# Performance work log

Hardware: AMD Instinct MI355X
Metric: run time of the kernel (lower is better)

Reference implementation:

```python
import jax, jax.numpy as jnp
import numpy as np

R = 3                 # corr_radius
STRIDE = 4
RES = (384, 512)      # model_resolution (H, W)
G = 2 * R + 1         # 7: support grid side


def setup_inputs() -> dict:
    key = jax.random.key(0)
    ks = jax.random.split(key, 16)
    B, S, N, C = 1, 8, 1024, 128
    H0, W0 = RES[0] // STRIDE, RES[1] // STRIDE  # 96, 128
    inp = {}
    for i in range(4):
        h, w = H0 >> i, W0 >> i
        inp[f"fmaps{i}"] = jax.random.normal(ks[i], (B, S, C, h, w), jnp.float32)
        inp[f"track{i}"] = jax.random.normal(ks[4 + i], (B, G * G, N, C), jnp.float32)
    inp["coords"] = jax.random.uniform(ks[8], (B, S, N, 2), jnp.float32) * jnp.asarray([W0 - 1.0, H0 - 1.0], jnp.float32)
    inp["vis"] = jax.random.normal(ks[9], (B, S, N, 1), jnp.float32)
    inp["conf"] = jax.random.normal(ks[10], (B, S, N, 1), jnp.float32)
    r2 = G * G
    inp["w1"] = jax.random.normal(ks[11], (r2 * r2, 384), jnp.float32) * (1.0 / np.sqrt(r2 * r2))
    inp["b1"] = jnp.zeros((384,), jnp.float32)
    inp["w2"] = jax.random.normal(ks[12], (384, 256), jnp.float32) * (1.0 / np.sqrt(384))
    inp["b2"] = jnp.zeros((256,), jnp.float32)
    inp["time_emb"] = jax.random.normal(ks[13], (1, S, 1110), jnp.float32) * 0.02
    return inp


def bilinear_sample(fmap, x, y):
    """fmap: (BT, C, H, W); x, y: (BT, M) pixel coords. Border padding, align_corners=True
    (matches torch grid_sample as used by co-tracker's bilinear_sampler)."""
    BT, C, H, W = fmap.shape
    x0f = jnp.floor(x)
    y0f = jnp.floor(y)
    wx = (x - x0f)[:, None, :]
    wy = (y - y0f)[:, None, :]
    x0 = jnp.clip(x0f.astype(jnp.int32), 0, W - 1)
    x1 = jnp.clip(x0f.astype(jnp.int32) + 1, 0, W - 1)
    y0 = jnp.clip(y0f.astype(jnp.int32), 0, H - 1)
    y1 = jnp.clip(y0f.astype(jnp.int32) + 1, 0, H - 1)
    flat = fmap.reshape(BT, C, H * W)

    def g(yi, xi):
        idx = (yi * W + xi)[:, None, :]  # (BT, 1, M)
        return jnp.take_along_axis(flat, idx, axis=2)  # (BT, C, M)

    return (g(y0, x0) * (1 - wx) * (1 - wy) + g(y0, x1) * wx * (1 - wy)
            + g(y1, x0) * (1 - wx) * wy + g(y1, x1) * wx * wy)


def posenc(x, min_deg=0, max_deg=10):
    scales = jnp.asarray([2.0 ** i for i in range(min_deg, max_deg)], x.dtype)
    xb = (x[..., None, :] * scales[:, None]).reshape(x.shape[:-1] + (-1,))
    four = jnp.sin(jnp.concatenate([xb, xb + 0.5 * jnp.pi], axis=-1))
    return jnp.concatenate([x, four], axis=-1)


def reference(fmaps0, fmaps1, fmaps2, fmaps3, track0, track1, track2, track3,
              coords, vis, conf, w1, b1, w2, b2, time_emb):
    B, S, N, _ = coords.shape
    fps = [fmaps0, fmaps1, fmaps2, fmaps3]
    tps = [track0, track1, track2, track3]
    d = jnp.linspace(-R, R, G)
    xoff, yoff = jnp.meshgrid(d, d, indexing='ij')  # (7,7): rows = x offset, cols = y offset

    embs = []
    for lvl in range(4):
        fm = fps[lvl]
        C, H, W = fm.shape[2], fm.shape[3], fm.shape[4]
        c = coords.reshape(B * S, N, 1, 1, 2) / (2.0 ** lvl)
        x = c[..., 0] + xoff          # (B*S, N, 7, 7)
        y = c[..., 1] + yoff
        M = N * G * G
        sampled = bilinear_sample(fm.reshape(B * S, C, H, W), x.reshape(B * S, M), y.reshape(B * S, M))
        corr_feat = sampled.reshape(B, S, C, N, G, G).transpose(0, 1, 3, 4, 5, 2)  # (B,S,N,7,7,C)
        track = tps[lvl].reshape(B, G, G, N, C).transpose(0, 3, 1, 2, 4)           # (B,N,7,7,C)
        vol = jnp.einsum('btnhwc,bnijc->btnhwij', corr_feat, track)                # (B,S,N,7,7,7,7)
        h = jax.nn.gelu(vol.reshape(B * S * N, G * G * G * G) @ w1 + b1, approximate=False)
        embs.append(h @ w2 + b2)
    corr_embs = jnp.concatenate(embs, axis=-1).reshape(B, S, N, -1)  # (B,S,N,1024)

    rel_f = jnp.pad(coords[:, :-1] - coords[:, 1:], ((0, 0), (0, 1), (0, 0), (0, 0)))
    rel_b = jnp.pad(coords[:, 1:] - coords[:, :-1], ((0, 0), (1, 0), (0, 0), (0, 0)))
    scale = jnp.asarray([RES[1], RES[0]], jnp.float32) / STRIDE
    rel_emb = posenc(jnp.concatenate([rel_f / scale, rel_b / scale], axis=-1))  # (B,S,N,84)

    x = jnp.concatenate([vis, conf, corr_embs, rel_emb], axis=-1)  # (B,S,N,1110)
    x = x.transpose(0, 2, 1, 3).reshape(B * N, S, -1) + time_emb
    return x.reshape(B, N, S, -1)
```

## Files before the change

kernel.cpp:

```cpp
#include <hip/hip_runtime.h>
#include <math.h>


#define SN 8
#define NN 1024
#define CC 128
#define K1P2 2752
#define H1 384
#define H2 256
#define DOUT 1110

typedef short bf16x8 __attribute__((ext_vector_type(8)));
typedef short s16x4 __attribute__((ext_vector_type(4)));
typedef float f32x4 __attribute__((ext_vector_type(4)));

__device__ inline unsigned short f2b(float x) {
    union { float f; unsigned u; } v; v.f = x;
    unsigned r = v.u + 0x7FFFu + ((v.u >> 16) & 1u);
    return (unsigned short)(r >> 16);
}
__device__ inline float b2f(unsigned short u) {
    union { unsigned u; float f; } v; v.u = (unsigned)u << 16; return v.f;
}
__device__ inline void gll16(const void* g, void* l) {
    __builtin_amdgcn_global_load_lds(
        (const __attribute__((address_space(1))) void*)g,
        (__attribute__((address_space(3))) void*)l, 16, 0, 0);
}
__device__ inline int swz(int row, int g) {
    return row * 128 + ((g ^ (row & 7)) << 3);
}

__global__ __launch_bounds__(256) void conv_fmap_kernel(
    const float* __restrict__ in, unsigned short* __restrict__ outp,
    int H, int W)
{
    const int Hp = H + 8, Wp = W + 8;
    const int s = blockIdx.x / Hp, yp = blockIdx.x % Hp;
    const int y = min(max(yp - 4, 0), H - 1);
    const float* src = in + (size_t)s * CC * H * W + (size_t)y * W;
    unsigned short* dst = outp + ((size_t)s * Hp + yp) * Wp * CC;
    for (int idx = threadIdx.x; idx < Wp * CC; idx += 256) {
        int xp = idx >> 7, c = idx & 127;
        int x = min(max(xp - 4, 0), W - 1);
        dst[idx] = f2b(src[(size_t)c * H * W + x]);
    }
}

__global__ __launch_bounds__(256, 3) void sample_vol_kernel(
    const unsigned short* __restrict__ fq0, const unsigned short* __restrict__ fq1,
    const unsigned short* __restrict__ fq2, const unsigned short* __restrict__ fq3,
    const float* __restrict__ tk0, const float* __restrict__ tk1,
    const float* __restrict__ tk2, const float* __restrict__ tk3,
    const float* __restrict__ coords,
    unsigned short* __restrict__ vol,
    int lv0)
{
    __shared__ __align__(16) unsigned short bufA[80 * 128];
    __shared__ __align__(16) unsigned short bufB[80 * 128];
    __shared__ __align__(16) unsigned short pcL[80 * 68];
    const int n = blockIdx.x & 1023, g = blockIdx.x >> 10;
    const int lvl = lv0 + g;
    const unsigned short* fpad = (lvl == 0) ? fq0 : (lvl == 1) ? fq1
                               : (lvl == 2) ? fq2 : fq3;
    const float* track = (lvl == 0) ? tk0 : (lvl == 1) ? tk1
                       : (lvl == 2) ? tk2 : tk3;
    const int Wp = (128 >> lvl) + 8;
    const int t = threadIdx.x;
    const int lane = t & 63, wv = t >> 6;
    const int rsub = lane & 15, kq = lane >> 4;
    const float inv = 1.0f / (float)(1 << lvl);
    const size_t plane = (size_t)((96 >> lvl) + 8) * Wp * CC;

    int poff[5], ldso[5];
    #pragma unroll
    for (int i = 0; i < 5; ++i) {
        int task64 = wv * 5 + i;
        int point = task64 * 4 + (lane >> 4);
        int v = point / 10, xs = point - v * 10;
        int j = (lane & 15) ^ (point & 7);
        poff[i] = (v * Wp + xs) * CC + j * 8;
        ldso[i] = task64 * 512;
    }

    float cxa[SN], cya[SN];
    int fxa[SN], fya[SN], ea[SN];
    #pragma unroll
    for (int s = 0; s < SN; ++s) {
        float2 c2 = *(const float2*)&coords[((size_t)s * NN + n) * 2];
        cxa[s] = c2.x * inv; cya[s] = c2.y * inv;
        fxa[s] = (int)floorf(cxa[s]);
        fya[s] = (int)floorf(cya[s]);
        ea[s] = (fxa[s] - 3) & ~1;
    }

    int p0b[2], ij0a[2], tau8[2]; bool vld[2];
    #pragma unroll
    for (int rep = 0; rep < 2; ++rep) {
        int tau = t + rep * 256;
        vld[rep] = (tau < 343);
        int tt = vld[rep] ? tau : 0;
        int ab = tt / 7, blk = tt - 7 * ab;
        int a = ab / 7, b = ab - 7 * a;
        p0b[rep] = b * 10 + a;
        ij0a[rep] = blk * 8;
        tau8[rep] = tt * 8;
    }

    {
        const unsigned short* base =
            fpad + ((fya[0] + 1) * Wp + (ea[0] + 4)) * CC;
        #pragma unroll
        for (int i = 0; i < 5; ++i) gll16(base + poff[i], &bufA[ldso[i]]);
    }
    for (int task = t; task < 49 * 16; task += 256) {
        int row = task >> 4, gg = task & 15;
        const float* srcp = &track[((size_t)row * NN + n) * CC + gg * 8];
        float4 f0 = *(const float4*)srcp;
        float4 f1 = *(const float4*)(srcp + 4);
        bf16x8 v8;
        v8[0] = f2b(f0.x); v8[1] = f2b(f0.y); v8[2] = f2b(f0.z); v8[3] = f2b(f0.w);
        v8[4] = f2b(f1.x); v8[5] = f2b(f1.y); v8[6] = f2b(f1.z); v8[7] = f2b(f1.w);
        *(bf16x8*)&bufB[swz(row, gg)] = v8;
    }
    {
        unsigned* T32 = (unsigned*)bufB;
        for (int i = t; i < 15 * 64; i += 256) T32[49 * 64 + i] = 0;
    }
    asm volatile("s_waitcnt lgkmcnt(0)" ::: "memory");
    __builtin_amdgcn_sched_barrier(0);
    __builtin_amdgcn_s_barrier();
    bf16x8 tf[4];
    #pragma unroll
    for (int kk = 0; kk < 4; ++kk)
        tf[kk] = *(const bf16x8*)&bufB[swz(wv * 16 + rsub, kk * 4 + kq)];
    asm volatile("s_waitcnt lgkmcnt(0)" ::: "memory");
    __builtin_amdgcn_sched_barrier(0);
    __builtin_amdgcn_s_barrier();
    __builtin_amdgcn_sched_barrier(0);
    {
        const unsigned short* base =
            fpad + plane + ((fya[1] + 1) * Wp + (ea[1] + 4)) * CC;
        #pragma unroll
        for (int i = 0; i < 5; ++i) gll16(base + poff[i], &bufB[ldso[i]]);
    }

    #pragma unroll
    for (int sl = 0; sl < SN; ++sl) {
        unsigned short* pbuf = (sl & 1) ? bufB : bufA;
        const float wx = cxa[sl] - (float)fxa[sl], wy = cya[sl] - (float)fya[sl];
        const float w00 = (1.f - wx) * (1.f - wy), w10 = wx * (1.f - wy);
        const float w01 = (1.f - wx) * wy,         w11 = wx * wy;
        const int off = fxa[sl] - 3 - ea[sl];

        if (sl == 0) {
            asm volatile("s_waitcnt vmcnt(5) lgkmcnt(0)" ::: "memory");
        } else if (sl == 1) {
            if (wv < 2) asm volatile("s_waitcnt vmcnt(7) lgkmcnt(0)" ::: "memory");
            else        asm volatile("s_waitcnt vmcnt(6) lgkmcnt(0)" ::: "memory");
        } else if (sl == SN - 1) {
            if (wv < 2) asm volatile("s_waitcnt vmcnt(4) lgkmcnt(0)" ::: "memory");
            else        asm volatile("s_waitcnt vmcnt(2) lgkmcnt(0)" ::: "memory");
        } else {
            if (wv < 2) asm volatile("s_waitcnt vmcnt(9) lgkmcnt(0)" ::: "memory");
            else        asm volatile("s_waitcnt vmcnt(7) lgkmcnt(0)" ::: "memory");
        }
        __builtin_amdgcn_sched_barrier(0);
        __builtin_amdgcn_s_barrier();
        __builtin_amdgcn_sched_barrier(0);

        {
            f32x4 acc[5] = {};
            __builtin_amdgcn_s_setprio(1);
            #pragma unroll
            for (int kk = 0; kk < 4; ++kk) {
                int gg = kk * 4 + kq;
                #pragma unroll
                for (int ti = 0; ti < 5; ++ti) {
                    bf16x8 a = *(const bf16x8*)&pbuf[swz(ti * 16 + rsub, gg)];
                    acc[ti] = __builtin_amdgcn_mfma_f32_16x16x32_bf16(a, tf[kk], acc[ti], 0, 0, 0);
                }
            }
            __builtin_amdgcn_s_setprio(0);
            const int col = wv * 16 + rsub;
            #pragma unroll
            for (int ti = 0; ti < 5; ++ti)
                #pragma unroll
                for (int r = 0; r < 4; ++r)
                    pcL[(ti * 16 + kq * 4 + r) * 68 + col] = f2b(acc[ti][r]);
        }
        asm volatile("s_waitcnt lgkmcnt(0)" ::: "memory");
        __builtin_amdgcn_s_barrier();
        __builtin_amdgcn_sched_barrier(0);

        if (sl + 2 < SN) {
            const unsigned short* base =
                fpad + (size_t)(sl + 2) * plane
                + ((fya[sl + 2] + 1) * Wp + (ea[sl + 2] + 4)) * CC;
            #pragma unroll
            for (int i = 0; i < 5; ++i) gll16(base + poff[i], &pbuf[ldso[i]]);
        }
        __builtin_amdgcn_sched_barrier(0);

        {
            unsigned short* vrow = vol + ((size_t)(g * SN + sl) * NN + n) * K1P2;
            #pragma unroll
            for (int rep = 0; rep < 2; ++rep) {
                if (vld[rep]) {
                    int base = (p0b[rep] + off) * 68 + ij0a[rep];
                    s16x4 a0 = *(const s16x4*)&pcL[base],       a1 = *(const s16x4*)&pcL[base + 4];
                    s16x4 b0 = *(const s16x4*)&pcL[base + 68],  b1 = *(const s16x4*)&pcL[base + 72];
                    s16x4 c0 = *(const s16x4*)&pcL[base + 680], c1 = *(const s16x4*)&pcL[base + 684];
                    s16x4 d0 = *(const s16x4*)&pcL[base + 748], d1 = *(const s16x4*)&pcL[base + 752];
                    unsigned w[4];
                    #pragma unroll
                    for (int j = 0; j < 4; ++j) {
                        const int e0 = 2 * j, e1 = 2 * j + 1;
                        float v0 = w00 * b2f((unsigned short)(e0 < 4 ? a0[e0 & 3] : a1[e0 & 3]))
                                 + w10 * b2f((unsigned short)(e0 < 4 ? b0[e0 & 3] : b1[e0 & 3]))
                                 + w01 * b2f((unsigned short)(e0 < 4 ? c0[e0 & 3] : c1[e0 & 3]))
                                 + w11 * b2f((unsigned short)(e0 < 4 ? d0[e0 & 3] : d1[e0 & 3]));
                        float v1 = w00 * b2f((unsigned short)(e1 < 4 ? a0[e1 & 3] : a1[e1 & 3]))
                                 + w10 * b2f((unsigned short)(e1 < 4 ? b0[e1 & 3] : b1[e1 & 3]))
                                 + w01 * b2f((unsigned short)(e1 < 4 ? c0[e1 & 3] : c1[e1 & 3]))
                                 + w11 * b2f((unsigned short)(e1 < 4 ? d0[e1 & 3] : d1[e1 & 3]));
                        w[j] = (unsigned)f2b(v0) | ((unsigned)f2b(v1) << 16);
                    }
                    uint4 st; st.x = w[0]; st.y = w[1]; st.z = w[2]; st.w = w[3];
                    *(uint4*)(vrow + tau8[rep]) = st;
                }
            }
        }
    }
}

__global__ __launch_bounds__(256) void zpad_kernel(
    unsigned short* __restrict__ vol, int rows)
{
    int r = blockIdx.x * 256 + threadIdx.x;
    if (r < rows) {
        uint4 z; z.x = 0; z.y = 0; z.z = 0; z.w = 0;
        *(uint4*)(vol + (size_t)r * K1P2 + 2744) = z;
    }
}

__global__ __launch_bounds__(256) void conv_w1_kernel(
    const float* __restrict__ w1, unsigned short* __restrict__ w1t)
{
    __shared__ float tile[32][33];
    const int kb = blockIdx.x * 32, nb = blockIdx.y * 32;
    const int tx = threadIdx.x & 31, ty = threadIdx.x >> 5;
    #pragma unroll
    for (int i = 0; i < 32; i += 8) {
        int kp = kb + ty + i;
        int k = -1;
        if (kp < 2744) {
            int tau = kp >> 3, r = kp & 7;
            int ab = tau / 7, blk = tau - 7 * ab;
            int ij = blk * 8 + r;
            if (ij < 49) k = ab * 49 + ij;
        }
        tile[ty + i][tx] = (k >= 0) ? w1[(size_t)k * H1 + nb + tx] : 0.f;
    }
    __syncthreads();
    #pragma unroll
    for (int i = 0; i < 32; i += 8)
        w1t[(size_t)(nb + ty + i) * K1P2 + kb + tx] = f2b(tile[tx][ty + i]);
}

__global__ __launch_bounds__(256, 3) void gemm1_kernel(
    const unsigned short* __restrict__ A,
    const unsigned short* __restrict__ Bt,
    const float* __restrict__ bias,
    unsigned short* __restrict__ Hout)
{
    __shared__ __align__(16) unsigned short As[3 * 128 * 32];
    __shared__ __align__(16) unsigned short Bs[3 * 128 * 32];
    const int h = blockIdx.x, q = gridDim.x >> 3;
    const int l = (h & 7) * q + (h >> 3);
    const int m0 = (l / 3) * 128, n0 = (l % 3) * 128;
    const int t = threadIdx.x, lane = t & 63, wv = t >> 6;
    const int wm = wv >> 1, wn = wv & 1;
    const int rsub = lane & 15, kq = lane >> 4;

    const int rA0 = t >> 2, sA0 = (t & 3) ^ ((rA0 >> 1) & 3);
    const int rA1 = (t + 256) >> 2, sA1 = ((t + 256) & 3) ^ ((rA1 >> 1) & 3);
    const unsigned short* gA0 = A  + (size_t)(m0 + rA0) * K1P2 + sA0 * 8;
    const unsigned short* gA1 = A  + (size_t)(m0 + rA1) * K1P2 + sA1 * 8;
    const unsigned short* gB0 = Bt + (size_t)(n0 + rA0) * K1P2 + sA0 * 8;
    const unsigned short* gB1 = Bt + (size_t)(n0 + rA1) * K1P2 + sA1 * 8;
    const int chunk0 = (t & ~63) * 8, chunk1 = (256 + (t & ~63)) * 8;

    f32x4 acc[4][4] = {};

    const int NSTEP = K1P2 / 32;
    #pragma unroll
    for (int p = 0; p < 2; ++p) {
        size_t ko = (size_t)p * 32;
        int lb = p * 4096;
        gll16(gA0 + ko, &As[lb + chunk0]); gll16(gA1 + ko, &As[lb + chunk1]);
        gll16(gB0 + ko, &Bs[lb + chunk0]); gll16(gB1 + ko, &Bs[lb + chunk1]);
    }
    int cur = 0, nxt = 2;
    for (int st = 0; st < NSTEP; ++st) {
        if (st + 1 < NSTEP) asm volatile("s_waitcnt vmcnt(4)" ::: "memory");
        else                asm volatile("s_waitcnt vmcnt(0)" ::: "memory");
        __builtin_amdgcn_s_barrier();
        __builtin_amdgcn_sched_barrier(0);
        if (st + 2 < NSTEP) {
            size_t ko = (size_t)(st + 2) * 32;
            int lb = nxt * 4096;
            gll16(gA0 + ko, &As[lb + chunk0]);
            gll16(gA1 + ko, &As[lb + chunk1]);
            gll16(gB0 + ko, &Bs[lb + chunk0]);
            gll16(gB1 + ko, &Bs[lb + chunk1]);
        }
        const int lb = cur * 4096;
        bf16x8 af[4], bfr[4];
        #pragma unroll
        for (int mi = 0; mi < 4; ++mi) {
            int r = wm * 64 + mi * 16 + rsub;
            int phys = r * 4 + (kq ^ ((r >> 1) & 3));
            af[mi] = *(const bf16x8*)&As[lb + phys * 8];
        }
        #pragma unroll
        for (int ni = 0; ni < 4; ++ni) {
            int r = wn * 64 + ni * 16 + rsub;
            int phys = r * 4 + (kq ^ ((r >> 1) & 3));
            bfr[ni] = *(const bf16x8*)&Bs[lb + phys * 8];
        }
        __builtin_amdgcn_s_setprio(1);
        #pragma unroll
        for (int mi = 0; mi < 4; ++mi)
            #pragma unroll
            for (int ni = 0; ni < 4; ++ni)
                acc[mi][ni] = __builtin_amdgcn_mfma_f32_16x16x32_bf16(
                    af[mi], bfr[ni], acc[mi][ni], 0, 0, 0);
        __builtin_amdgcn_s_setprio(0);
        cur = (cur == 2) ? 0 : cur + 1;
        nxt = (nxt == 2) ? 0 : nxt + 1;
    }
    #pragma unroll
    for (int mi = 0; mi < 4; ++mi) {
        int row = m0 + wm * 64 + mi * 16 + kq * 4;
        #pragma unroll
        for (int ni = 0; ni < 4; ++ni) {
            int col = n0 + wn * 64 + ni * 16 + rsub;
            float bcol = bias[col];
            #pragma unroll
            for (int r = 0; r < 4; ++r) {
                float x = acc[mi][ni][r] + bcol;
                float gg = 0.5f * x * (1.f + erff(x * 0.70710678118654752f));
                Hout[(size_t)(row + r) * H1 + col] = f2b(gg);
            }
        }
    }
}

__global__ __launch_bounds__(256, 3) void gemm2_kernel(
    const unsigned short* __restrict__ A,
    const unsigned short* __restrict__ Bt,
    const float* __restrict__ bias,
    const float* __restrict__ te,
    float* __restrict__ out,
    int lv0)
{
    __shared__ __align__(16) unsigned short As[3 * 128 * 32];
    __shared__ __align__(16) unsigned short Bs[3 * 128 * 32];
    const int h = blockIdx.x, q = gridDim.x >> 3;
    const int l = (h & 7) * q + (h >> 3);
    const int m0 = (l >> 1) * 128, n0 = (l & 1) * 128;
    const int t = threadIdx.x, lane = t & 63, wv = t >> 6;
    const int wm = wv >> 1, wn = wv & 1;
    const int rsub = lane & 15, kq = lane >> 4;

    const int rA0 = t >> 2, sA0 = (t & 3) ^ ((rA0 >> 1) & 3);
    const int rA1 = (t + 256) >> 2, sA1 = ((t + 256) & 3) ^ ((rA1 >> 1) & 3);
    const unsigned short* gA0 = A  + (size_t)(m0 + rA0) * H1 + sA0 * 8;
    const unsigned short* gA1 = A  + (size_t)(m0 + rA1) * H1 + sA1 * 8;
    const unsigned short* gB0 = Bt + (size_t)(n0 + rA0) * H1 + sA0 * 8;
    const unsigned short* gB1 = Bt + (size_t)(n0 + rA1) * H1 + sA1 * 8;
    const int chunk0 = (t & ~63) * 8, chunk1 = (256 + (t & ~63)) * 8;

    f32x4 acc[4][4] = {};

    const int NSTEP = H1 / 32;
    #pragma unroll
    for (int p = 0; p < 2; ++p) {
        size_t ko = (size_t)p * 32;
        int lb = p * 4096;
        gll16(gA0 + ko, &As[lb + chunk0]); gll16(gA1 + ko, &As[lb + chunk1]);
        gll16(gB0 + ko, &Bs[lb + chunk0]); gll16(gB1 + ko, &Bs[lb + chunk1]);
    }
    int cur = 0, nxt = 2;
    for (int st = 0; st < NSTEP; ++st) {
        if (st + 1 < NSTEP) asm volatile("s_waitcnt vmcnt(4)" ::: "memory");
        else                asm volatile("s_waitcnt vmcnt(0)" ::: "memory");
        __builtin_amdgcn_s_barrier();
        __builtin_amdgcn_sched_barrier(0);
        if (st + 2 < NSTEP) {
            size_t ko = (size_t)(st + 2) * 32;
            int lb = nxt * 4096;
            gll16(gA0 + ko, &As[lb + chunk0]);
            gll16(gA1 + ko, &As[lb + chunk1]);
            gll16(gB0 + ko, &Bs[lb + chunk0]);
            gll16(gB1 + ko, &Bs[lb + chunk1]);
        }
        const int lb = cur * 4096;
        bf16x8 af[4], bfr[4];
        #pragma unroll
        for (int mi = 0; mi < 4; ++mi) {
            int r = wm * 64 + mi * 16 + rsub;
            int phys = r * 4 + (kq ^ ((r >> 1) & 3));
            af[mi] = *(const bf16x8*)&As[lb + phys * 8];
        }
        #pragma unroll
        for (int ni = 0; ni < 4; ++ni) {
            int r = wn * 64 + ni * 16 + rsub;
            int phys = r * 4 + (kq ^ ((r >> 1) & 3));
            bfr[ni] = *(const bf16x8*)&Bs[lb + phys * 8];
        }
        __builtin_amdgcn_s_setprio(1);
        #pragma unroll
        for (int mi = 0; mi < 4; ++mi)
            #pragma unroll
            for (int ni = 0; ni < 4; ++ni)
                acc[mi][ni] = __builtin_amdgcn_mfma_f32_16x16x32_bf16(
                    af[mi], bfr[ni], acc[mi][ni], 0, 0, 0);
        __builtin_amdgcn_s_setprio(0);
        cur = (cur == 2) ? 0 : cur + 1;
        nxt = (nxt == 2) ? 0 : nxt + 1;
    }
    #pragma unroll
    for (int mi = 0; mi < 4; ++mi) {
        int rowb = m0 + wm * 64 + mi * 16 + kq * 4;
        #pragma unroll
        for (int ni = 0; ni < 4; ++ni) {
            int col = n0 + wn * 64 + ni * 16 + rsub;
            float bcol = bias[col];
            #pragma unroll
            for (int r = 0; r < 4; ++r) {
                int row = rowb + r;
                int g = row >> 13, s = (row >> 10) & 7, n = row & 1023;
                int dcol = 2 + (lv0 + g) * H2 + col;
                out[((size_t)n * SN + s) * DOUT + dcol] =
                    acc[mi][ni][r] + bcol + te[s * DOUT + dcol];
            }
        }
    }
}

__global__ __launch_bounds__(256) void conv_t_kernel(
    const float* __restrict__ in, unsigned short* __restrict__ outp,
    int K, int Nw, int Kp)
{
    __shared__ float tile[32][33];
    const int kb = blockIdx.x * 32, nb = blockIdx.y * 32;
    const int tx = threadIdx.x & 31, ty = threadIdx.x >> 5;
    #pragma unroll
    for (int i = 0; i < 32; i += 8) {
        int k = kb + ty + i, nn = nb + tx;
        tile[ty + i][tx] = (k < K && nn < Nw) ? in[(size_t)k * Nw + nn] : 0.f;
    }
    __syncthreads();
    #pragma unroll
    for (int i = 0; i < 32; i += 8) {
        int nn = nb + ty + i, k = kb + tx;
        if (nn < Nw) outp[(size_t)nn * Kp + k] = f2b(tile[tx][ty + i]);
    }
}

__global__ __launch_bounds__(128) void tail_kernel(
    const float* __restrict__ coords, const float* __restrict__ vis,
    const float* __restrict__ conf, const float* __restrict__ te,
    float* __restrict__ out)
{
    const int b = blockIdx.x;
    const int n = b >> 3, s = b & 7;
    const int d = threadIdx.x;
    if (d >= 86) return;
    const size_t ob = (size_t)b * DOUT;
    if (d == 0) {
        out[ob + 0] = vis[(size_t)s * NN + n] + te[s * DOUT + 0];
    } else if (d == 1) {
        out[ob + 1] = conf[(size_t)s * NN + n] + te[s * DOUT + 1];
    } else {
        int rd = d - 2;
        float cx = coords[((size_t)s * NN + n) * 2 + 0];
        float cy = coords[((size_t)s * NN + n) * 2 + 1];
        float rfx = 0.f, rfy = 0.f, rbx = 0.f, rby = 0.f;
        if (s < SN - 1) {
            rfx = cx - coords[((size_t)(s + 1) * NN + n) * 2 + 0];
            rfy = cy - coords[((size_t)(s + 1) * NN + n) * 2 + 1];
        }
        if (s > 0) {
            rbx = cx - coords[((size_t)(s - 1) * NN + n) * 2 + 0];
            rby = cy - coords[((size_t)(s - 1) * NN + n) * 2 + 1];
        }
        float r4[4] = {rfx / 128.f, rfy / 96.f, rbx / 128.f, rby / 96.f};
        float val;
        if (rd < 4) {
            val = r4[rd];
        } else if (rd < 44) {
            int q = rd - 4; int deg = q >> 2, comp = q & 3;
            val = sinf(r4[comp] * (float)(1 << deg));
        } else {
            int q = rd - 44; int deg = q >> 2, comp = q & 3;
            val = sinf(r4[comp] * (float)(1 << deg) + 1.57079632679489662f);
        }
        int od = 1026 + rd;
        out[ob + od] = val + te[s * DOUT + od];
    }
}

extern "C" void kernel_launch(void* const* d_in, const int* in_sizes, int n_in,
                              void* d_out, int out_size, void* d_ws, size_t ws_size,
                              hipStream_t stream) {
    const float* fmaps[4] = {(const float*)d_in[0], (const float*)d_in[2],
                             (const float*)d_in[4], (const float*)d_in[6]};
    const float* track[4] = {(const float*)d_in[1], (const float*)d_in[3],
                             (const float*)d_in[5], (const float*)d_in[7]};
    const float* coords = (const float*)d_in[8];
    const float* vis    = (const float*)d_in[9];
    const float* conf   = (const float*)d_in[10];
    const float* w1     = (const float*)d_in[11];
    const float* b1     = (const float*)d_in[12];
    const float* w2     = (const float*)d_in[13];
    const float* b2     = (const float*)d_in[14];
    const float* te     = (const float*)d_in[15];
    float* out = (float*)d_out;

    const int Hs[4] = {96, 48, 24, 12};
    const int Ws[4] = {128, 64, 32, 16};

    char* wsb = (char*)d_ws;
    unsigned short* w1t = (unsigned short*)wsb;
    size_t off = (size_t)H1 * K1P2 * 2;
    unsigned short* w2t = (unsigned short*)(wsb + off);
    off += (size_t)H2 * H1 * 2;
    unsigned short* fpad[4];
    for (int l = 0; l < 4; ++l) {
        fpad[l] = (unsigned short*)(wsb + off);
        off += (size_t)SN * (Hs[l] + 8) * (Ws[l] + 8) * CC * 2;
    }
    off += 512;
    const size_t fixed = off;
    int n_lv = 4;
    while (n_lv > 1 &&
           fixed + (size_t)n_lv * SN * NN * (K1P2 + H1) * 2 > ws_size)
        n_lv >>= 1;
    unsigned short* volb = (unsigned short*)(wsb + fixed);
    unsigned short* hb   = volb + (size_t)n_lv * SN * NN * K1P2;

    conv_w1_kernel<<<dim3(K1P2 / 32, H1 / 32), 256, 0, stream>>>(w1, w1t);
    conv_t_kernel<<<dim3(H1 / 32, H2 / 32), 256, 0, stream>>>(w2, w2t, H1, H2, H1);
    for (int l = 0; l < 4; ++l)
        conv_fmap_kernel<<<SN * (Hs[l] + 8), 256, 0, stream>>>(
            fmaps[l], fpad[l], Hs[l], Ws[l]);
    zpad_kernel<<<(n_lv * SN * NN + 255) / 256, 256, 0, stream>>>(
        volb, n_lv * SN * NN);

    for (int lv0 = 0; lv0 < 4; lv0 += n_lv) {
        sample_vol_kernel<<<n_lv * NN, 256, 0, stream>>>(
            fpad[0], fpad[1], fpad[2], fpad[3],
            track[0], track[1], track[2], track[3],
            coords, volb, lv0);
        const int rows = n_lv * SN * NN;
        gemm1_kernel<<<(rows / 128) * 3, 256, 0, stream>>>(volb, w1t, b1, hb);
        gemm2_kernel<<<(rows / 128) * 2, 256, 0, stream>>>(hb, w2t, b2, te, out, lv0);
    }
    tail_kernel<<<SN * NN, 128, 0, stream>>>(coords, vis, conf, te, out);
}
```

Before: 343.4 us.

## Repartition sample_vol MFMA work across five waves with track tiles held in registers

```diff
diff --git a/kernel.cpp b/kernel.cpp
--- a/kernel.cpp
+++ b/kernel.cpp
@@ -47,7 +47,7 @@
     }
 }
 
-__global__ __launch_bounds__(256, 3) void sample_vol_kernel(
+__global__ __launch_bounds__(320, 4) void sample_vol_kernel(
     const unsigned short* __restrict__ fq0, const unsigned short* __restrict__ fq1,
     const unsigned short* __restrict__ fq2, const unsigned short* __restrict__ fq3,
     const float* __restrict__ tk0, const float* __restrict__ tk1,
@@ -72,10 +72,10 @@
     const float inv = 1.0f / (float)(1 << lvl);
     const size_t plane = (size_t)((96 >> lvl) + 8) * Wp * CC;
 
-    int poff[5], ldso[5];
-    #pragma unroll
-    for (int i = 0; i < 5; ++i) {
-        int task64 = wv * 5 + i;
+    int poff[4], ldso[4];
+    #pragma unroll
+    for (int i = 0; i < 4; ++i) {
+        int task64 = wv * 4 + i;
         int point = task64 * 4 + (lane >> 4);
         int v = point / 10, xs = point - v * 10;
         int j = (lane & 15) ^ (point & 7);
@@ -97,7 +97,7 @@
     int p0b[2], ij0a[2], tau8[2]; bool vld[2];
     #pragma unroll
     for (int rep = 0; rep < 2; ++rep) {
-        int tau = t + rep * 256;
+        int tau = t + rep * 320;
         vld[rep] = (tau < 343);
         int tt = vld[rep] ? tau : 0;
         int ab = tt / 7, blk = tt - 7 * ab;
@@ -111,9 +111,9 @@
         const unsigned short* base =
             fpad + ((fya[0] + 1) * Wp + (ea[0] + 4)) * CC;
         #pragma unroll
-        for (int i = 0; i < 5; ++i) gll16(base + poff[i], &bufA[ldso[i]]);
-    }
-    for (int task = t; task < 49 * 16; task += 256) {
+        for (int i = 0; i < 4; ++i) gll16(base + poff[i], &bufA[ldso[i]]);
+    }
+    for (int task = t; task < 49 * 16; task += 320) {
         int row = task >> 4, gg = task & 15;
         const float* srcp = &track[((size_t)row * NN + n) * CC + gg * 8];
         float4 f0 = *(const float4*)srcp;
@@ -125,15 +125,17 @@
     }
     {
         unsigned* T32 = (unsigned*)bufB;
-        for (int i = t; i < 15 * 64; i += 256) T32[49 * 64 + i] = 0;
+        for (int i = t; i < 15 * 64; i += 320) T32[49 * 64 + i] = 0;
     }
     asm volatile("s_waitcnt lgkmcnt(0)" ::: "memory");
     __builtin_amdgcn_sched_barrier(0);
     __builtin_amdgcn_s_barrier();
-    bf16x8 tf[4];
-    #pragma unroll
-    for (int kk = 0; kk < 4; ++kk)
-        tf[kk] = *(const bf16x8*)&bufB[swz(wv * 16 + rsub, kk * 4 + kq)];
+    bf16x8 trkReg[4][4];
+    #pragma unroll
+    for (int ni = 0; ni < 4; ++ni)
+        #pragma unroll
+        for (int kk = 0; kk < 4; ++kk)
+            trkReg[ni][kk] = *(const bf16x8*)&bufB[swz(ni * 16 + rsub, kk * 4 + kq)];
     asm volatile("s_waitcnt lgkmcnt(0)" ::: "memory");
     __builtin_amdgcn_sched_barrier(0);
     __builtin_amdgcn_s_barrier();
@@ -142,7 +144,7 @@
         const unsigned short* base =
             fpad + plane + ((fya[1] + 1) * Wp + (ea[1] + 4)) * CC;
         #pragma unroll
-        for (int i = 0; i < 5; ++i) gll16(base + poff[i], &bufB[ldso[i]]);
+        for (int i = 0; i < 4; ++i) gll16(base + poff[i], &bufB[ldso[i]]);
     }
 
     #pragma unroll
@@ -154,40 +156,43 @@
         const int off = fxa[sl] - 3 - ea[sl];
 
         if (sl == 0) {
-            asm volatile("s_waitcnt vmcnt(5) lgkmcnt(0)" ::: "memory");
+            asm volatile("s_waitcnt vmcnt(0) lgkmcnt(0)" ::: "memory");
         } else if (sl == 1) {
-            if (wv < 2) asm volatile("s_waitcnt vmcnt(7) lgkmcnt(0)" ::: "memory");
-            else        asm volatile("s_waitcnt vmcnt(6) lgkmcnt(0)" ::: "memory");
+            if (wv == 0) asm volatile("s_waitcnt vmcnt(6) lgkmcnt(0)" ::: "memory");
+            else         asm volatile("s_waitcnt vmcnt(5) lgkmcnt(0)" ::: "memory");
         } else if (sl == SN - 1) {
-            if (wv < 2) asm volatile("s_waitcnt vmcnt(4) lgkmcnt(0)" ::: "memory");
-            else        asm volatile("s_waitcnt vmcnt(2) lgkmcnt(0)" ::: "memory");
+            if (wv == 0) asm volatile("s_waitcnt vmcnt(4) lgkmcnt(0)" ::: "memory");
+            else         asm volatile("s_waitcnt vmcnt(2) lgkmcnt(0)" ::: "memory");
         } else {
-            if (wv < 2) asm volatile("s_waitcnt vmcnt(9) lgkmcnt(0)" ::: "memory");
-            else        asm volatile("s_waitcnt vmcnt(7) lgkmcnt(0)" ::: "memory");
+            if (wv == 0) asm volatile("s_waitcnt vmcnt(8) lgkmcnt(0)" ::: "memory");
+            else         asm volatile("s_waitcnt vmcnt(6) lgkmcnt(0)" ::: "memory");
         }
         __builtin_amdgcn_sched_barrier(0);
         __builtin_amdgcn_s_barrier();
         __builtin_amdgcn_sched_barrier(0);
 
         {
-            f32x4 acc[5] = {};
+            f32x4 acc[4] = {};
             __builtin_amdgcn_s_setprio(1);
             #pragma unroll
             for (int kk = 0; kk < 4; ++kk) {
-                int gg = kk * 4 + kq;
+                bf16x8 pf = *(const bf16x8*)&pbuf[swz(wv * 16 + rsub, kk * 4 + kq)];
                 #pragma unroll
-                for (int ti = 0; ti < 5; ++ti) {
-                    bf16x8 a = *(const bf16x8*)&pbuf[swz(ti * 16 + rsub, gg)];
-                    acc[ti] = __builtin_amdgcn_mfma_f32_16x16x32_bf16(a, tf[kk], acc[ti], 0, 0, 0);
-                }
+                for (int ni = 0; ni < 4; ++ni)
+                    acc[ni] = __builtin_amdgcn_mfma_f32_16x16x32_bf16(
+                        trkReg[ni][kk], pf, acc[ni], 0, 0, 0);
             }
             __builtin_amdgcn_s_setprio(0);
-            const int col = wv * 16 + rsub;
-            #pragma unroll
-            for (int ti = 0; ti < 5; ++ti)
-                #pragma unroll
-                for (int r = 0; r < 4; ++r)
-                    pcL[(ti * 16 + kq * 4 + r) * 68 + col] = f2b(acc[ti][r]);
+            const int prow = wv * 16 + rsub;
+            #pragma unroll
+            for (int ni = 0; ni < 4; ++ni) {
+                s16x4 w4;
+                w4[0] = (short)f2b(acc[ni][0]);
+                w4[1] = (short)f2b(acc[ni][1]);
+                w4[2] = (short)f2b(acc[ni][2]);
+                w4[3] = (short)f2b(acc[ni][3]);
+                *(s16x4*)&pcL[prow * 68 + ni * 16 + kq * 4] = w4;
+            }
         }
         asm volatile("s_waitcnt lgkmcnt(0)" ::: "memory");
         __builtin_amdgcn_s_barrier();
@@ -198,7 +203,7 @@
                 fpad + (size_t)(sl + 2) * plane
                 + ((fya[sl + 2] + 1) * Wp + (ea[sl + 2] + 4)) * CC;
             #pragma unroll
-            for (int i = 0; i < 5; ++i) gll16(base + poff[i], &pbuf[ldso[i]]);
+            for (int i = 0; i < 4; ++i) gll16(base + poff[i], &pbuf[ldso[i]]);
         }
         __builtin_amdgcn_sched_barrier(0);
 
@@ -561,7 +566,7 @@
         volb, n_lv * SN * NN);
 
     for (int lv0 = 0; lv0 < 4; lv0 += n_lv) {
-        sample_vol_kernel<<<n_lv * NN, 256, 0, stream>>>(
+        sample_vol_kernel<<<n_lv * NN, 320, 0, stream>>>(
             fpad[0], fpad[1], fpad[2], fpad[3],
             track[0], track[1], track[2], track[3],
             coords, volb, lv0);
```

Result: slower. 476.5 us (+38.8%).
